# Kernel tuning notes

Hardware: AMD Instinct MI355X
Metric: run time of the kernel (lower is better)

The kernel has to match this reference:

```python
import jax, jax.numpy as jnp
import numpy as np

N = 50000
E = 800000
HID = 128
HEADS = 3
OPH = (HID + HEADS - 1) // HEADS  # 43
MID = OPH * HEADS                 # 129
OUT = 6


def _gat_layer(x, src, dst, W, a_src, a_dst, b, heads, ch, concat, num_nodes):
    # x: [N, F_in]; W: [F_in, heads*ch]; a_src/a_dst: [heads, ch]; b: [heads*ch] or [ch]
    h = (x @ W).reshape(num_nodes, heads, ch)          # [N, H, C]
    al = jnp.einsum('nhc,hc->nh', h, a_src)            # [N, H]
    ar = jnp.einsum('nhc,hc->nh', h, a_dst)            # [N, H]
    e = jax.nn.leaky_relu(al[src] + ar[dst], 0.2)      # [E, H]
    emax = jax.ops.segment_max(e, dst, num_segments=num_nodes)
    emax = jnp.where(jnp.isfinite(emax), emax, 0.0)
    ex = jnp.exp(e - emax[dst])                        # [E, H]
    denom = jax.ops.segment_sum(ex, dst, num_segments=num_nodes)
    alpha = ex / (denom[dst] + 1e-16)                  # [E, H]
    msg = h[src] * alpha[:, :, None]                   # [E, H, C]
    out = jax.ops.segment_sum(msg, dst, num_segments=num_nodes)  # [N, H, C]
    out = out.reshape(num_nodes, heads * ch) if concat else out.mean(axis=1)
    return out + b


def setup_inputs() -> dict:
    key = jax.random.key(0)
    ks = jax.random.split(key, 16)
    x = jax.random.normal(ks[0], (N, HID), dtype=jnp.float32)
    edge_index = jax.random.randint(ks[1], (2, E), 0, N, dtype=jnp.int64)
    s = 0.1
    return {
        'x': x, 'edge_index': edge_index,
        'W0': jax.random.normal(ks[2], (HID, HEADS * OPH), jnp.float32) * s,
        'a0s': jax.random.normal(ks[3], (HEADS, OPH), jnp.float32) * s,
        'a0d': jax.random.normal(ks[4], (HEADS, OPH), jnp.float32) * s,
        'b0': jnp.zeros((HEADS * OPH,), jnp.float32),
        'W1': jax.random.normal(ks[5], (MID, HEADS * OPH), jnp.float32) * s,
        'a1s': jax.random.normal(ks[6], (HEADS, OPH), jnp.float32) * s,
        'a1d': jax.random.normal(ks[7], (HEADS, OPH), jnp.float32) * s,
        'b1': jnp.zeros((HEADS * OPH,), jnp.float32),
        'W2': jax.random.normal(ks[8], (MID, OUT), jnp.float32) * s,
        'a2s': jax.random.normal(ks[9], (1, OUT), jnp.float32) * s,
        'a2d': jax.random.normal(ks[10], (1, OUT), jnp.float32) * s,
        'b2': jnp.zeros((OUT,), jnp.float32),
    }


def reference(x, edge_index, W0, a0s, a0d, b0, W1, a1s, a1d, b1, W2, a2s, a2d, b2):
    # add self loops (GATConv add_self_loops=True)
    loops = jnp.arange(N, dtype=edge_index.dtype)
    src = jnp.concatenate([edge_index[0], loops])
    dst = jnp.concatenate([edge_index[1], loops])
    h = _gat_layer(x, src, dst, W0, a0s, a0d, b0, HEADS, OPH, True, N)
    h = jax.nn.leaky_relu(h, 0.2)
    h = _gat_layer(h, src, dst, W1, a1s, a1d, b1, HEADS, OPH, True, N)
    h = jax.nn.leaky_relu(h, 0.2)
    out = _gat_layer(h, src, dst, W2, a2s, a2d, b2, 1, OUT, False, N)
    return out
```

## Files before the change

### kernel.cpp

```cpp
#include <hip/hip_runtime.h>

#define N_NODES 50000
#define N_EDGES 800000
#define ET (N_EDGES + N_NODES)
#define MID 129
#define OUTC 6
#define NB 196
#define CT 4096

typedef _Float16 half2v __attribute__((ext_vector_type(2)));
typedef _Float16 half8  __attribute__((ext_vector_type(8)));
typedef float    floatx4 __attribute__((ext_vector_type(4)));

__device__ __forceinline__ float lrelu(float x) { return fmaxf(x, 0.2f * x); }


__global__ void ccount_kernel(const int* __restrict__ dst, int* __restrict__ ccnt) {
    __shared__ int lh[NB];
    for (int i = threadIdx.x; i < NB; i += 256) lh[i] = 0;
    __syncthreads();
    int base = blockIdx.x * CT;
#pragma unroll 4
    for (int j = 0; j < CT; j += 256) {
        int e = base + j + threadIdx.x;
        if (e < ET) {
            int d = (e < N_EDGES) ? dst[e] : (e - N_EDGES);
            atomicAdd(&lh[d >> 8], 1);
        }
    }
    __syncthreads();
    for (int i = threadIdx.x; i < NB; i += 256) {
        int v = lh[i];
        if (v) atomicAdd(&ccnt[i], v);
    }
}

__global__ void cscan_kernel(const int* __restrict__ ccnt, int* __restrict__ cbase,
                             int* __restrict__ ccur) {
    __shared__ int buf[256];
    int t = threadIdx.x;
    buf[t] = (t < NB) ? ccnt[t] : 0;
    __syncthreads();
    for (int off = 1; off < 256; off <<= 1) {
        int v = (t >= off) ? buf[t - off] : 0;
        __syncthreads();
        buf[t] += v;
        __syncthreads();
    }
    int excl = t ? buf[t - 1] : 0;
    if (t < NB) { cbase[t] = excl; ccur[t] = excl; }
    if (t == NB - 1) cbase[NB] = buf[t];
}

__global__ void cscatter_kernel(const int* __restrict__ src, const int* __restrict__ dst,
                                int* __restrict__ ccur, unsigned int* __restrict__ cval) {
    __shared__ unsigned int staged[CT];
    __shared__ int lh[NB], lex[NB], lcur[NB], lgb[NB];
    __shared__ int sbuf[256];
    int tid = threadIdx.x;
    for (int i = tid; i < NB; i += 256) lh[i] = 0;
    __syncthreads();
    int base = blockIdx.x * CT;
    unsigned int myv[16];
    int myb[16];
    int myn = 0;
#pragma unroll
    for (int j = 0; j < 16; ++j) {
        int e = base + j * 256 + tid;
        if (e < ET) {
            int s, d;
            if (e < N_EDGES) { s = src[e]; d = dst[e]; }
            else             { s = d = e - N_EDGES; }
            int b = d >> 8;
            myv[j] = ((unsigned)b << 24) | ((unsigned)(d & 255) << 16) | (unsigned)s;
            myb[j] = b;
            atomicAdd(&lh[b], 1);
            myn = j + 1;
        }
    }
    __syncthreads();
    sbuf[tid] = (tid < NB) ? lh[tid] : 0;
    __syncthreads();
    for (int off = 1; off < 256; off <<= 1) {
        int v = (tid >= off) ? sbuf[tid - off] : 0;
        __syncthreads();
        sbuf[tid] += v;
        __syncthreads();
    }
    if (tid < NB) {
        int excl = tid ? sbuf[tid - 1] : 0;
        lex[tid] = excl;
        lcur[tid] = excl;
    }
    __syncthreads();
    for (int j = 0; j < myn; ++j) {
        int p = atomicAdd(&lcur[myb[j]], 1);
        staged[p] = myv[j];
    }
    __syncthreads();
    if (tid < NB) {
        int c = lh[tid];
        lgb[tid] = c ? atomicAdd(&ccur[tid], c) : 0;
    }
    __syncthreads();
    int tot = ET - base; if (tot > CT) tot = CT;
    for (int i = tid; i < tot; i += 256) {
        unsigned int v = staged[i];
        int b = v >> 24;
        cval[lgb[b] + (i - lex[b])] = v;
    }
}

__global__ __launch_bounds__(512)
void fine_kernel(const unsigned int* __restrict__ cval, const int* __restrict__ cbase,
                 int* __restrict__ rowp, unsigned short* __restrict__ csr_src) {
    __shared__ int h[256], cur[256], sb[256];
    int b = blockIdx.x;
    int beg = cbase[b], end = cbase[b + 1];
    int t = threadIdx.x;
    if (t < 256) h[t] = 0;
    __syncthreads();
    for (int i = beg + t; i < end; i += 512)
        atomicAdd(&h[(cval[i] >> 16) & 255], 1);
    __syncthreads();
    if (t < 256) sb[t] = h[t];
    __syncthreads();
    for (int off = 1; off < 256; off <<= 1) {
        int v = 0;
        if (t < 256 && t >= off) v = sb[t - off];
        __syncthreads();
        if (t < 256) sb[t] += v;
        __syncthreads();
    }
    if (t < 256) {
        int excl = t ? sb[t - 1] : 0;
        cur[t] = excl;
        int dstv = (b << 8) + t;
        if (dstv <= N_NODES) rowp[dstv] = beg + excl;
    }
    __syncthreads();
    for (int i = beg + t; i < end; i += 512) {
        unsigned int v = cval[i];
        int low = (v >> 16) & 255;
        int p = atomicAdd(&cur[low], 1);
        csr_src[beg + p] = (unsigned short)(v & 0xFFFFu);
    }
}

__global__ void padw_kernel(const float* __restrict__ W0, const float* __restrict__ a0s,
                            const float* __restrict__ a0d, const float* __restrict__ W1,
                            const float* __restrict__ a1s, const float* __restrict__ a1d,
                            _Float16* __restrict__ Wt0, _Float16* __restrict__ Wt1,
                            float* __restrict__ w128row1) {
    const int SEG = 144 * 128;
    int i = blockIdx.x * blockDim.x + threadIdx.x;
    if (i < 2 * SEG) {
        int l = i / SEG;
        int ii = i - l * SEG;
        int n = ii >> 7, k = ii & 127;
        const float* W = l ? W1 : W0;
        const float* as = l ? a1s : a0s;
        const float* ad = l ? a1d : a0d;
        float v = 0.f;
        if (n < 129) v = W[k * MID + n];
        else if (n < 132) {
            int h = n - 129;
            float sum = 0.f;
            for (int c = 0; c < 43; ++c) sum += W[k * MID + 43 * h + c] * as[43 * h + c];
            v = sum;
        } else if (n < 135) {
            int h = n - 132;
            float sum = 0.f;
            for (int c = 0; c < 43; ++c) sum += W[k * MID + 43 * h + c] * ad[43 * h + c];
            v = sum;
        }
        (l ? Wt1 : Wt0)[ii] = (_Float16)v;
    } else if (i < 2 * SEG + 144) {
        int n = i - 2 * SEG;
        float v = 0.f;
        if (n < 129) v = W1[128 * MID + n];
        else if (n < 132) {
            int h = n - 129;
            float sum = 0.f;
            for (int c = 0; c < 43; ++c) sum += W1[128 * MID + 43 * h + c] * a1s[43 * h + c];
            v = sum;
        } else if (n < 135) {
            int h = n - 132;
            float sum = 0.f;
            for (int c = 0; c < 43; ++c) sum += W1[128 * MID + 43 * h + c] * a1d[43 * h + c];
            v = sum;
        }
        w128row1[n] = v;
    }
}

template <bool SRC32, bool RANK1>
__global__ __launch_bounds__(256)
void gemm_mfma_kernel(const float* __restrict__ X32, const _Float16* __restrict__ Xh,
                      const float* __restrict__ Xl,
                      const _Float16* __restrict__ Wt, const float* __restrict__ w128,
                      _Float16* __restrict__ Hm16, float* __restrict__ Hl,
                      float* __restrict__ al4, float* __restrict__ ar4) {
    int wave = threadIdx.x >> 6, lane = threadIdx.x & 63;
    int mt = blockIdx.x * 4 + wave;
    if (mt * 16 >= N_NODES) return;
    int t = lane & 15, quad = lane >> 4;
    int row0 = mt * 16;

    half8 af[4];
    if (SRC32) {
        const float* arow = X32 + ((size_t)(row0 + t) << 7) + quad * 8;
#pragma unroll
        for (int kt = 0; kt < 4; ++kt) {
            float4 a0 = *(const float4*)(arow + kt * 32);
            float4 a1 = *(const float4*)(arow + kt * 32 + 4);
            half8 h;
            h[0] = (_Float16)a0.x; h[1] = (_Float16)a0.y;
            h[2] = (_Float16)a0.z; h[3] = (_Float16)a0.w;
            h[4] = (_Float16)a1.x; h[5] = (_Float16)a1.y;
            h[6] = (_Float16)a1.z; h[7] = (_Float16)a1.w;
            af[kt] = h;
        }
    } else {
        const _Float16* arow = Xh + ((size_t)(row0 + t) << 7) + quad * 8;
#pragma unroll
        for (int kt = 0; kt < 4; ++kt) af[kt] = *(const half8*)(arow + kt * 32);
    }

    floatx4 acc[3];
#pragma unroll
    for (int nt = 0; nt < 3; ++nt) {
        int ntile = blockIdx.y * 3 + nt;
        const _Float16* brow = Wt + ((size_t)(ntile * 16 + t) << 7) + quad * 8;
        floatx4 a = {0.f, 0.f, 0.f, 0.f};
#pragma unroll
        for (int kt = 0; kt < 4; ++kt) {
            half8 b = *(const half8*)(brow + kt * 32);
            a = __builtin_amdgcn_mfma_f32_16x16x32_f16(af[kt], b, a, 0, 0, 0);
        }
        acc[nt] = a;
    }

#pragma unroll
    for (int r = 0; r < 4; ++r) {
        int row = row0 + quad * 4 + r;
        float xl = RANK1 ? Xl[row] : 0.f;
#pragma unroll
        for (int nt = 0; nt < 3; ++nt) {
            int n = (blockIdx.y * 3 + nt) * 16 + t;
            float v = acc[nt][r];
            if (RANK1) v += xl * w128[n];
            if (n < 128) {
                Hm16[((size_t)row << 7) + n] = (_Float16)v;
            } else if (n == 128) {
                Hl[row] = v;
            } else if (n < 132) {
                al4[row * 4 + (n - 129)] = v;
            } else if (n < 135) {
                ar4[row * 4 + (n - 132)] = v;
            }
        }
    }
}

template <bool ACT, bool L2EPI>
__global__ void agg129_kernel(const _Float16* __restrict__ Hm16, const float* __restrict__ Hl,
                              const float* __restrict__ al4, const float* __restrict__ ar4,
                              const int* __restrict__ rowp, const unsigned short* __restrict__ srcs,
                              const float* __restrict__ bias, _Float16* __restrict__ Omh,
                              float* __restrict__ Ol,
                              const float* __restrict__ W2, const float* __restrict__ a2s,
                              const float* __restrict__ a2d, float* __restrict__ H2,
                              float* __restrict__ al2, float* __restrict__ ar2) {
    __shared__ float4 exs[4][4][17];
    int lane = threadIdx.x & 63;
    int wv   = threadIdx.x >> 6;
    int qd   = lane >> 4;
    int q    = lane & 15;
    int wid  = ((blockIdx.x * 4 + wv) << 2) + qd;
    bool active = wid < N_NODES;
    int widc = active ? wid : 0;

    int beg = 0, end = 0;
    if (active) { beg = rowp[wid]; end = rowp[wid + 1]; }
    float4 arv = *(const float4*)(ar4 + (size_t)widc * 4);
    float ard0 = arv.x, ard1 = arv.y, ard2 = arv.z;

    int cb = 8 * q;
    bool bm0[8], bm1[8];
#pragma unroll
    for (int j = 0; j < 8; ++j) {
        bm0[j] = (cb + j) < 43;
        bm1[j] = (cb + j) < 86;
    }
    unsigned selv[4];
#pragma unroll
    for (int p = 0; p < 4; ++p) {
        int c0 = cb + 2 * p, c1 = c0 + 1;
        int l0 = (c0 < 43) ? 4 : (c0 < 86) ? 6 : 0;
        int l1 = (c1 < 43) ? 4 : (c1 < 86) ? 6 : 0;
        selv[p] = (unsigned)l0 | ((unsigned)(l0 + 1) << 8) |
                  ((unsigned)l1 << 16) | ((unsigned)(l1 + 1) << 24);
    }

    float accv[8];
#pragma unroll
    for (int j = 0; j < 8; ++j) accv[j] = 0.f;
    float acc128 = 0.f;
    float s0 = 0.f, s1 = 0.f, s2 = 0.f;
    float4* exq = exs[wv][qd];

    for (int base = beg; base < end; base += 16) {
        int i = base + q;
        float e0 = 0.f, e1 = 0.f, e2 = 0.f;
        int s = 0;
        if (i < end) {
            s = (int)srcs[i];
            float4 av = *(const float4*)(al4 + (size_t)s * 4);
            e0 = __expf(lrelu(av.x + ard0));
            e1 = __expf(lrelu(av.y + ard1));
            e2 = __expf(lrelu(av.z + ard2));
            s0 += e0; s1 += e1; s2 += e2;
        }
        exq[q] = make_float4(e0, e1, e2, __int_as_float(s));
        int cnt = end - base; if (cnt > 16) cnt = 16;
        for (int t = 0; t < cnt; ++t) {
            float4 ed = exq[t];
            int ss = __float_as_int(ed.w);
            half8 hv = *(const half8*)(Hm16 + ((size_t)ss << 7) + cb);
            unsigned p01 = __builtin_bit_cast(unsigned, __builtin_amdgcn_cvt_pkrtz(ed.x, ed.y));
            unsigned p2z = __builtin_bit_cast(unsigned, __builtin_amdgcn_cvt_pkrtz(ed.z, ed.z));
            if (q == 0) acc128 += ed.z * Hl[ss];
#pragma unroll
            for (int p = 0; p < 4; ++p) {
                unsigned wp = __builtin_amdgcn_perm(p01, p2z, selv[p]);
                half2v w2 = __builtin_bit_cast(half2v, wp);
                accv[2 * p]     += (float)w2[0] * (float)hv[2 * p];
                accv[2 * p + 1] += (float)w2[1] * (float)hv[2 * p + 1];
            }
        }
    }
#pragma unroll
    for (int off = 1; off < 16; off <<= 1) {
        s0 += __shfl_xor(s0, off, 64);
        s1 += __shfl_xor(s1, off, 64);
        s2 += __shfl_xor(s2, off, 64);
    }
    float d0 = 1.f / (s0 + 1e-16f);
    float d1 = 1.f / (s1 + 1e-16f);
    float d2 = 1.f / (s2 + 1e-16f);

    float4 bv0 = *(const float4*)(bias + cb);
    float4 bv1 = *(const float4*)(bias + cb + 4);
    float bb[8] = {bv0.x, bv0.y, bv0.z, bv0.w, bv1.x, bv1.y, bv1.z, bv1.w};
    float o[8];
#pragma unroll
    for (int j = 0; j < 8; ++j) {
        float dv = bm0[j] ? d0 : (bm1[j] ? d1 : d2);
        o[j] = accv[j] * dv + bb[j];
        if (ACT) o[j] = lrelu(o[j]);
    }
    float o128 = 0.f;
    if (q == 0) {
        o128 = acc128 * d2 + bias[128];
        if (ACT) o128 = lrelu(o128);
    }
    if (!L2EPI) {
        if (active) {
            half8 oh;
#pragma unroll
            for (int j = 0; j < 8; ++j) oh[j] = (_Float16)o[j];
            *(half8*)(Omh + ((size_t)wid << 7) + cb) = oh;
            if (q == 0) Ol[wid] = o128;
        }
    } else {
        float pr[OUTC];
#pragma unroll
        for (int c = 0; c < OUTC; ++c) pr[c] = 0.f;
#pragma unroll
        for (int j = 0; j < 8; ++j) {
            const float* wr = W2 + (cb + j) * OUTC;
            float ov = o[j];
#pragma unroll
            for (int c = 0; c < OUTC; ++c) pr[c] += ov * wr[c];
        }
        if (q == 0) {
#pragma unroll
            for (int c = 0; c < OUTC; ++c) pr[c] += o128 * W2[128 * OUTC + c];
        }
#pragma unroll
        for (int off = 1; off < 16; off <<= 1)
#pragma unroll
            for (int c = 0; c < OUTC; ++c) pr[c] += __shfl_xor(pr[c], off, 64);
        if (active && q == 0) {
            float sl = 0.f, sr = 0.f;
#pragma unroll
            for (int c = 0; c < OUTC; ++c) {
                H2[wid * OUTC + c] = pr[c];
                sl += pr[c] * a2s[c];
                sr += pr[c] * a2d[c];
            }
            al2[wid] = sl;
            ar2[wid] = sr;
        }
    }
}

__global__ void agg6_kernel(const float* __restrict__ H2, const float* __restrict__ al2,
                            const float* __restrict__ ar2, const int* __restrict__ rowp,
                            const unsigned short* __restrict__ srcs, const float* __restrict__ b2,
                            float* __restrict__ out) {
    __shared__ float2 exs[4][8][9];
    int lane = threadIdx.x & 63;
    int wv   = threadIdx.x >> 6;
    int g8   = lane >> 3;
    int c    = lane & 7;
    int wid  = ((blockIdx.x * 4 + wv) << 3) + g8;
    bool active = wid < N_NODES;
    int widc = active ? wid : 0;
    int beg = 0, end = 0;
    if (active) { beg = rowp[wid]; end = rowp[wid + 1]; }
    float ard = ar2[widc];
    int cc = (c < OUTC) ? c : 0;
    float ssum = 0.f, acc = 0.f;
    float2* exq = exs[wv][g8];
    for (int base = beg; base < end; base += 8) {
        int i = base + c;
        float ex = 0.f;
        int s = 0;
        if (i < end) {
            s = (int)srcs[i];
            ex = __expf(lrelu(al2[s] + ard));
            ssum += ex;
        }
        exq[c] = make_float2(ex, __int_as_float(s));
        int cnt = end - base; if (cnt > 8) cnt = 8;
        for (int t = 0; t < cnt; ++t) {
            float2 ed = exq[t];
            int ss = __float_as_int(ed.y);
            acc += ed.x * H2[ss * OUTC + cc];
        }
    }
#pragma unroll
    for (int off = 1; off < 8; off <<= 1) ssum += __shfl_xor(ssum, off, 64);
    float dinv = 1.f / (ssum + 1e-16f);
    if (active && c < OUTC) out[(size_t)wid * OUTC + c] = acc * dinv + b2[c];
}


extern "C" void kernel_launch(void* const* d_in, const int* in_sizes, int n_in,
                              void* d_out, int out_size, void* d_ws, size_t ws_size,
                              hipStream_t stream) {
    const float* x   = (const float*)d_in[0];
    const int*   ei  = (const int*)d_in[1];
    const float* W0  = (const float*)d_in[2];
    const float* a0s = (const float*)d_in[3];
    const float* a0d = (const float*)d_in[4];
    const float* b0  = (const float*)d_in[5];
    const float* W1  = (const float*)d_in[6];
    const float* a1s = (const float*)d_in[7];
    const float* a1d = (const float*)d_in[8];
    const float* b1  = (const float*)d_in[9];
    const float* W2  = (const float*)d_in[10];
    const float* a2s = (const float*)d_in[11];
    const float* a2d = (const float*)d_in[12];
    const float* b2  = (const float*)d_in[13];
    float* out = (float*)d_out;

    char* p = (char*)d_ws;
    auto take = [&](size_t bytes) -> void* {
        void* r = (void*)p;
        p += (bytes + 255) & ~(size_t)255;
        return r;
    };
    int*            ccnt     = (int*)take((size_t)NB * 4);
    int*            cbase    = (int*)take((size_t)(NB + 1) * 4);
    int*            ccur     = (int*)take((size_t)NB * 4);
    unsigned int*   cval     = (unsigned int*)take((size_t)ET * 4);
    int*            rowp     = (int*)take((size_t)(N_NODES + 1) * 4);
    unsigned short* csr_src  = (unsigned short*)take((size_t)ET * 2);
    float*          al4      = (float*)take((size_t)N_NODES * 4 * 4);
    float*          ar4      = (float*)take((size_t)N_NODES * 4 * 4);
    _Float16*       Hm16     = (_Float16*)take((size_t)N_NODES * 128 * 2);
    _Float16*       Omh      = (_Float16*)take((size_t)N_NODES * 128 * 2);
    float*          Hl       = (float*)take((size_t)N_NODES * 4);
    float*          Ol       = (float*)take((size_t)N_NODES * 4);
    _Float16*       Wt0      = (_Float16*)take((size_t)144 * 128 * 2);
    _Float16*       Wt1      = (_Float16*)take((size_t)144 * 128 * 2);
    float*          w128row1 = (float*)take((size_t)144 * 4);
    float*          H2       = (float*)take((size_t)N_NODES * OUTC * 4);
    float*          al2      = (float*)take((size_t)N_NODES * 4);
    float*          ar2      = (float*)take((size_t)N_NODES * 4);

    const int* esrc = ei;
    const int* edst = ei + N_EDGES;

    hipMemsetAsync(ccnt, 0, (size_t)NB * 4, stream);
    const int cgrid = (ET + CT - 1) / CT;
    ccount_kernel<<<cgrid, 256, 0, stream>>>(edst, ccnt);
    cscan_kernel<<<1, 256, 0, stream>>>(ccnt, cbase, ccur);
    cscatter_kernel<<<cgrid, 256, 0, stream>>>(esrc, edst, ccur, cval);
    fine_kernel<<<NB, 512, 0, stream>>>(cval, cbase, rowp, csr_src);

    padw_kernel<<<(2 * 144 * 128 + 144 + 255) / 256, 256, 0, stream>>>(
        W0, a0s, a0d, W1, a1s, a1d, Wt0, Wt1, w128row1);

    const dim3 gemm_grid((N_NODES / 16 + 3) / 4, 3);
    const int  agg129_grid = (N_NODES + 15) / 16;
    const int  agg6_grid   = (N_NODES + 31) / 32;

    gemm_mfma_kernel<true, false><<<gemm_grid, 256, 0, stream>>>(
        x, (const _Float16*)nullptr, Ol, Wt0, w128row1, Hm16, Hl, al4, ar4);
    agg129_kernel<true, false><<<agg129_grid, 256, 0, stream>>>(
        Hm16, Hl, al4, ar4, rowp, csr_src, b0, Omh, Ol,
        nullptr, nullptr, nullptr, nullptr, nullptr, nullptr);

    gemm_mfma_kernel<false, true><<<gemm_grid, 256, 0, stream>>>(
        (const float*)nullptr, Omh, Ol, Wt1, w128row1, Hm16, Hl, al4, ar4);
    agg129_kernel<true, true><<<agg129_grid, 256, 0, stream>>>(
        Hm16, Hl, al4, ar4, rowp, csr_src, b1, (_Float16*)nullptr, (float*)nullptr,
        W2, a2s, a2d, H2, al2, ar2);

    agg6_kernel<<<agg6_grid, 256, 0, stream>>>(H2, al2, ar2, rowp, csr_src, b2, out);
}
```

Baseline: 280.5 us.

## Fuse independent preprocessing kernels and unroll aggregation gather loops

Merges the edge-count kernel with the weight-padding kernel, and the coarse scatter kernel with the first-layer GEMM, into single launches whose blocks branch on block index, so independent work shares a launch and can overlap. This removes two kernel launches and the serialization between them. It also unrolls the per-edge gather loops in the 129-wide and 6-wide aggregation kernels by 4 and 2, issuing several neighbor loads before the math to raise memory-level parallelism. The cost is more registers and shared memory in the fused kernels, which may lower occupancy.

```diff
diff --git a/kernel.cpp b/kernel.cpp
--- a/kernel.cpp
+++ b/kernel.cpp
@@ -7,6 +7,9 @@
 #define OUTC 6
 #define NB 196
 #define CT 4096
+#define CGRID ((ET + CT - 1) / CT)
+#define MTB ((N_NODES / 16 + 3) / 4)
+#define PADW_BLOCKS ((2 * 144 * 128 + 144 + 255) / 256)
 
 typedef _Float16 half2v __attribute__((ext_vector_type(2)));
 typedef _Float16 half8  __attribute__((ext_vector_type(8)));
@@ -14,146 +17,12 @@
 
 __device__ __forceinline__ float lrelu(float x) { return fmaxf(x, 0.2f * x); }
 
-
-__global__ void ccount_kernel(const int* __restrict__ dst, int* __restrict__ ccnt) {
-    __shared__ int lh[NB];
-    for (int i = threadIdx.x; i < NB; i += 256) lh[i] = 0;
-    __syncthreads();
-    int base = blockIdx.x * CT;
-#pragma unroll 4
-    for (int j = 0; j < CT; j += 256) {
-        int e = base + j + threadIdx.x;
-        if (e < ET) {
-            int d = (e < N_EDGES) ? dst[e] : (e - N_EDGES);
-            atomicAdd(&lh[d >> 8], 1);
-        }
-    }
-    __syncthreads();
-    for (int i = threadIdx.x; i < NB; i += 256) {
-        int v = lh[i];
-        if (v) atomicAdd(&ccnt[i], v);
-    }
-}
-
-__global__ void cscan_kernel(const int* __restrict__ ccnt, int* __restrict__ cbase,
-                             int* __restrict__ ccur) {
-    __shared__ int buf[256];
-    int t = threadIdx.x;
-    buf[t] = (t < NB) ? ccnt[t] : 0;
-    __syncthreads();
-    for (int off = 1; off < 256; off <<= 1) {
-        int v = (t >= off) ? buf[t - off] : 0;
-        __syncthreads();
-        buf[t] += v;
-        __syncthreads();
-    }
-    int excl = t ? buf[t - 1] : 0;
-    if (t < NB) { cbase[t] = excl; ccur[t] = excl; }
-    if (t == NB - 1) cbase[NB] = buf[t];
-}
-
-__global__ void cscatter_kernel(const int* __restrict__ src, const int* __restrict__ dst,
-                                int* __restrict__ ccur, unsigned int* __restrict__ cval) {
-    __shared__ unsigned int staged[CT];
-    __shared__ int lh[NB], lex[NB], lcur[NB], lgb[NB];
-    __shared__ int sbuf[256];
-    int tid = threadIdx.x;
-    for (int i = tid; i < NB; i += 256) lh[i] = 0;
-    __syncthreads();
-    int base = blockIdx.x * CT;
-    unsigned int myv[16];
-    int myb[16];
-    int myn = 0;
-#pragma unroll
-    for (int j = 0; j < 16; ++j) {
-        int e = base + j * 256 + tid;
-        if (e < ET) {
-            int s, d;
-            if (e < N_EDGES) { s = src[e]; d = dst[e]; }
-            else             { s = d = e - N_EDGES; }
-            int b = d >> 8;
-            myv[j] = ((unsigned)b << 24) | ((unsigned)(d & 255) << 16) | (unsigned)s;
-            myb[j] = b;
-            atomicAdd(&lh[b], 1);
-            myn = j + 1;
-        }
-    }
-    __syncthreads();
-    sbuf[tid] = (tid < NB) ? lh[tid] : 0;
-    __syncthreads();
-    for (int off = 1; off < 256; off <<= 1) {
-        int v = (tid >= off) ? sbuf[tid - off] : 0;
-        __syncthreads();
-        sbuf[tid] += v;
-        __syncthreads();
-    }
-    if (tid < NB) {
-        int excl = tid ? sbuf[tid - 1] : 0;
-        lex[tid] = excl;
-        lcur[tid] = excl;
-    }
-    __syncthreads();
-    for (int j = 0; j < myn; ++j) {
-        int p = atomicAdd(&lcur[myb[j]], 1);
-        staged[p] = myv[j];
-    }
-    __syncthreads();
-    if (tid < NB) {
-        int c = lh[tid];
-        lgb[tid] = c ? atomicAdd(&ccur[tid], c) : 0;
-    }
-    __syncthreads();
-    int tot = ET - base; if (tot > CT) tot = CT;
-    for (int i = tid; i < tot; i += 256) {
-        unsigned int v = staged[i];
-        int b = v >> 24;
-        cval[lgb[b] + (i - lex[b])] = v;
-    }
-}
-
-__global__ __launch_bounds__(512)
-void fine_kernel(const unsigned int* __restrict__ cval, const int* __restrict__ cbase,
-                 int* __restrict__ rowp, unsigned short* __restrict__ csr_src) {
-    __shared__ int h[256], cur[256], sb[256];
-    int b = blockIdx.x;
-    int beg = cbase[b], end = cbase[b + 1];
-    int t = threadIdx.x;
-    if (t < 256) h[t] = 0;
-    __syncthreads();
-    for (int i = beg + t; i < end; i += 512)
-        atomicAdd(&h[(cval[i] >> 16) & 255], 1);
-    __syncthreads();
-    if (t < 256) sb[t] = h[t];
-    __syncthreads();
-    for (int off = 1; off < 256; off <<= 1) {
-        int v = 0;
-        if (t < 256 && t >= off) v = sb[t - off];
-        __syncthreads();
-        if (t < 256) sb[t] += v;
-        __syncthreads();
-    }
-    if (t < 256) {
-        int excl = t ? sb[t - 1] : 0;
-        cur[t] = excl;
-        int dstv = (b << 8) + t;
-        if (dstv <= N_NODES) rowp[dstv] = beg + excl;
-    }
-    __syncthreads();
-    for (int i = beg + t; i < end; i += 512) {
-        unsigned int v = cval[i];
-        int low = (v >> 16) & 255;
-        int p = atomicAdd(&cur[low], 1);
-        csr_src[beg + p] = (unsigned short)(v & 0xFFFFu);
-    }
-}
-
-__global__ void padw_kernel(const float* __restrict__ W0, const float* __restrict__ a0s,
-                            const float* __restrict__ a0d, const float* __restrict__ W1,
-                            const float* __restrict__ a1s, const float* __restrict__ a1d,
-                            _Float16* __restrict__ Wt0, _Float16* __restrict__ Wt1,
-                            float* __restrict__ w128row1) {
+__device__ __forceinline__ void padw_body(int i, const float* __restrict__ W0,
+                                          const float* __restrict__ a0s, const float* __restrict__ a0d,
+                                          const float* __restrict__ W1, const float* __restrict__ a1s,
+                                          const float* __restrict__ a1d, _Float16* __restrict__ Wt0,
+                                          _Float16* __restrict__ Wt1, float* __restrict__ w128row1) {
     const int SEG = 144 * 128;
-    int i = blockIdx.x * blockDim.x + threadIdx.x;
     if (i < 2 * SEG) {
         int l = i / SEG;
         int ii = i - l * SEG;
@@ -174,7 +43,7 @@
             for (int c = 0; c < 43; ++c) sum += W[k * MID + 43 * h + c] * ad[43 * h + c];
             v = sum;
         }
-        (l ? Wt1 : Wt0)[ii] = (_Float16)v;
+        (l ? Wt1 : Wt0)[i - l * SEG] = (_Float16)v;
     } else if (i < 2 * SEG + 144) {
         int n = i - 2 * SEG;
         float v = 0.f;
@@ -194,15 +63,65 @@
     }
 }
 
+__global__ __launch_bounds__(256)
+void fused_count_padw_kernel(const int* __restrict__ dst, int* __restrict__ ccnt,
+                             const float* __restrict__ W0, const float* __restrict__ a0s,
+                             const float* __restrict__ a0d, const float* __restrict__ W1,
+                             const float* __restrict__ a1s, const float* __restrict__ a1d,
+                             _Float16* __restrict__ Wt0, _Float16* __restrict__ Wt1,
+                             float* __restrict__ w128row1) {
+    if ((int)blockIdx.x < CGRID) {
+        __shared__ int lh[NB];
+        for (int i = threadIdx.x; i < NB; i += 256) lh[i] = 0;
+        __syncthreads();
+        int base = blockIdx.x * CT;
+#pragma unroll 4
+        for (int j = 0; j < CT; j += 256) {
+            int e = base + j + threadIdx.x;
+            if (e < ET) {
+                int d = (e < N_EDGES) ? dst[e] : (e - N_EDGES);
+                atomicAdd(&lh[d >> 8], 1);
+            }
+        }
+        __syncthreads();
+        for (int i = threadIdx.x; i < NB; i += 256) {
+            int v = lh[i];
+            if (v) atomicAdd(&ccnt[i], v);
+        }
+    } else {
+        int i = ((int)blockIdx.x - CGRID) * 256 + threadIdx.x;
+        padw_body(i, W0, a0s, a0d, W1, a1s, a1d, Wt0, Wt1, w128row1);
+    }
+}
+
+__global__ void cscan_kernel(const int* __restrict__ ccnt, int* __restrict__ cbase,
+                             int* __restrict__ ccur) {
+    __shared__ int buf[256];
+    int t = threadIdx.x;
+    buf[t] = (t < NB) ? ccnt[t] : 0;
+    __syncthreads();
+    for (int off = 1; off < 256; off <<= 1) {
+        int v = (t >= off) ? buf[t - off] : 0;
+        __syncthreads();
+        buf[t] += v;
+        __syncthreads();
+    }
+    int excl = t ? buf[t - 1] : 0;
+    if (t < NB) { cbase[t] = excl; ccur[t] = excl; }
+    if (t == NB - 1) cbase[NB] = buf[t];
+}
+
 template <bool SRC32, bool RANK1>
-__global__ __launch_bounds__(256)
-void gemm_mfma_kernel(const float* __restrict__ X32, const _Float16* __restrict__ Xh,
-                      const float* __restrict__ Xl,
-                      const _Float16* __restrict__ Wt, const float* __restrict__ w128,
-                      _Float16* __restrict__ Hm16, float* __restrict__ Hl,
-                      float* __restrict__ al4, float* __restrict__ ar4) {
-    int wave = threadIdx.x >> 6, lane = threadIdx.x & 63;
-    int mt = blockIdx.x * 4 + wave;
+__device__ __forceinline__ void gemm_body(int mtb, int nyb, int tid,
+                                          const float* __restrict__ X32,
+                                          const _Float16* __restrict__ Xh,
+                                          const float* __restrict__ Xl,
+                                          const _Float16* __restrict__ Wt,
+                                          const float* __restrict__ w128,
+                                          _Float16* __restrict__ Hm16, float* __restrict__ Hl,
+                                          float* __restrict__ al4, float* __restrict__ ar4) {
+    int wave = tid >> 6, lane = tid & 63;
+    int mt = mtb * 4 + wave;
     if (mt * 16 >= N_NODES) return;
     int t = lane & 15, quad = lane >> 4;
     int row0 = mt * 16;
@@ -230,7 +149,7 @@
     floatx4 acc[3];
 #pragma unroll
     for (int nt = 0; nt < 3; ++nt) {
-        int ntile = blockIdx.y * 3 + nt;
+        int ntile = nyb * 3 + nt;
         const _Float16* brow = Wt + ((size_t)(ntile * 16 + t) << 7) + quad * 8;
         floatx4 a = {0.f, 0.f, 0.f, 0.f};
 #pragma unroll
@@ -247,7 +166,7 @@
         float xl = RANK1 ? Xl[row] : 0.f;
 #pragma unroll
         for (int nt = 0; nt < 3; ++nt) {
-            int n = (blockIdx.y * 3 + nt) * 16 + t;
+            int n = (nyb * 3 + nt) * 16 + t;
             float v = acc[nt][r];
             if (RANK1) v += xl * w128[n];
             if (n < 128) {
@@ -261,6 +180,122 @@
             }
         }
     }
+}
+
+__global__ __launch_bounds__(256)
+void fused_scatter_gemm0_kernel(const int* __restrict__ src, const int* __restrict__ dst,
+                                int* __restrict__ ccur, unsigned int* __restrict__ cval,
+                                const float* __restrict__ X32, const _Float16* __restrict__ Wt0,
+                                _Float16* __restrict__ Hm16, float* __restrict__ Hl,
+                                float* __restrict__ al4, float* __restrict__ ar4) {
+    if ((int)blockIdx.x < CGRID) {
+        __shared__ unsigned int staged[CT];
+        __shared__ int lh[NB], lex[NB], lcur[NB], lgb[NB];
+        __shared__ int sbuf[256];
+        int tid = threadIdx.x;
+        for (int i = tid; i < NB; i += 256) lh[i] = 0;
+        __syncthreads();
+        int base = blockIdx.x * CT;
+        unsigned int myv[16];
+        int myb[16];
+        int myn = 0;
+#pragma unroll
+        for (int j = 0; j < 16; ++j) {
+            int e = base + j * 256 + tid;
+            if (e < ET) {
+                int s, d;
+                if (e < N_EDGES) { s = src[e]; d = dst[e]; }
+                else             { s = d = e - N_EDGES; }
+                int b = d >> 8;
+                myv[j] = ((unsigned)b << 24) | ((unsigned)(d & 255) << 16) | (unsigned)s;
+                myb[j] = b;
+                atomicAdd(&lh[b], 1);
+                myn = j + 1;
+            }
+        }
+        __syncthreads();
+        sbuf[tid] = (tid < NB) ? lh[tid] : 0;
+        __syncthreads();
+        for (int off = 1; off < 256; off <<= 1) {
+            int v = (tid >= off) ? sbuf[tid - off] : 0;
+            __syncthreads();
+            sbuf[tid] += v;
+            __syncthreads();
+        }
+        if (tid < NB) {
+            int excl = tid ? sbuf[tid - 1] : 0;
+            lex[tid] = excl;
+            lcur[tid] = excl;
+        }
+        __syncthreads();
+        for (int j = 0; j < myn; ++j) {
+            int p = atomicAdd(&lcur[myb[j]], 1);
+            staged[p] = myv[j];
+        }
+        __syncthreads();
+        if (tid < NB) {
+            int c = lh[tid];
+            lgb[tid] = c ? atomicAdd(&ccur[tid], c) : 0;
+        }
+        __syncthreads();
+        int tot = ET - base; if (tot > CT) tot = CT;
+        for (int i = tid; i < tot; i += 256) {
+            unsigned int v = staged[i];
+            int b = v >> 24;
+            cval[lgb[b] + (i - lex[b])] = v;
+        }
+    } else {
+        int b = (int)blockIdx.x - CGRID;
+        int nyb = b / MTB;
+        int mtb = b - nyb * MTB;
+        gemm_body<true, false>(mtb, nyb, threadIdx.x, X32, nullptr, nullptr,
+                               Wt0, nullptr, Hm16, Hl, al4, ar4);
+    }
+}
+
+__global__ __launch_bounds__(512)
+void fine_kernel(const unsigned int* __restrict__ cval, const int* __restrict__ cbase,
+                 int* __restrict__ rowp, unsigned short* __restrict__ csr_src) {
+    __shared__ int h[256], cur[256], sb[256];
+    int b = blockIdx.x;
+    int beg = cbase[b], end = cbase[b + 1];
+    int t = threadIdx.x;
+    if (t < 256) h[t] = 0;
+    __syncthreads();
+    for (int i = beg + t; i < end; i += 512)
+        atomicAdd(&h[(cval[i] >> 16) & 255], 1);
+    __syncthreads();
+    if (t < 256) sb[t] = h[t];
+    __syncthreads();
+    for (int off = 1; off < 256; off <<= 1) {
+        int v = 0;
+        if (t < 256 && t >= off) v = sb[t - off];
+        __syncthreads();
+        if (t < 256) sb[t] += v;
+        __syncthreads();
+    }
+    if (t < 256) {
+        int excl = t ? sb[t - 1] : 0;
+        cur[t] = excl;
+        int dstv = (b << 8) + t;
+        if (dstv <= N_NODES) rowp[dstv] = beg + excl;
+    }
+    __syncthreads();
+    for (int i = beg + t; i < end; i += 512) {
+        unsigned int v = cval[i];
+        int low = (v >> 16) & 255;
+        int p = atomicAdd(&cur[low], 1);
+        csr_src[beg + p] = (unsigned short)(v & 0xFFFFu);
+    }
+}
+
+__global__ __launch_bounds__(256)
+void gemm1_kernel(const _Float16* __restrict__ Xh, const float* __restrict__ Xl,
+                  const _Float16* __restrict__ Wt, const float* __restrict__ w128,
+                  _Float16* __restrict__ Hm16, float* __restrict__ Hl,
+                  float* __restrict__ al4, float* __restrict__ ar4) {
+    gemm_body<false, true>(blockIdx.x, blockIdx.y, threadIdx.x, nullptr, Xh, Xl,
+                           Wt, w128, Hm16, Hl, al4, ar4);
 }
 
 template <bool ACT, bool L2EPI>
@@ -324,13 +359,44 @@
         }
         exq[q] = make_float4(e0, e1, e2, __int_as_float(s));
         int cnt = end - base; if (cnt > 16) cnt = 16;
-        for (int t = 0; t < cnt; ++t) {
+        int t = 0;
+        for (; t + 3 < cnt; t += 4) {
+            float4 ed[4];
+            int sx[4];
+            half8 hv[4];
+#pragma unroll
+            for (int u = 0; u < 4; ++u) ed[u] = exq[t + u];
+#pragma unroll
+            for (int u = 0; u < 4; ++u) {
+                sx[u] = __float_as_int(ed[u].w);
+                hv[u] = *(const half8*)(Hm16 + ((size_t)sx[u] << 7) + cb);
+            }
+            if (q == 0) {
+                acc128 += ed[0].z * Hl[sx[0]];
+                acc128 += ed[1].z * Hl[sx[1]];
+                acc128 += ed[2].z * Hl[sx[2]];
+                acc128 += ed[3].z * Hl[sx[3]];
+            }
+#pragma unroll
+            for (int u = 0; u < 4; ++u) {
+                unsigned p01 = __builtin_bit_cast(unsigned, __builtin_amdgcn_cvt_pkrtz(ed[u].x, ed[u].y));
+                unsigned p2z = __builtin_bit_cast(unsigned, __builtin_amdgcn_cvt_pkrtz(ed[u].z, ed[u].z));
+#pragma unroll
+                for (int p = 0; p < 4; ++p) {
+                    unsigned wp = __builtin_amdgcn_perm(p01, p2z, selv[p]);
+                    half2v w2 = __builtin_bit_cast(half2v, wp);
+                    accv[2 * p]     += (float)w2[0] * (float)hv[u][2 * p];
+                    accv[2 * p + 1] += (float)w2[1] * (float)hv[u][2 * p + 1];
+                }
+            }
+        }
+        for (; t < cnt; ++t) {
             float4 ed = exq[t];
             int ss = __float_as_int(ed.w);
             half8 hv = *(const half8*)(Hm16 + ((size_t)ss << 7) + cb);
+            if (q == 0) acc128 += ed.z * Hl[ss];
             unsigned p01 = __builtin_bit_cast(unsigned, __builtin_amdgcn_cvt_pkrtz(ed.x, ed.y));
             unsigned p2z = __builtin_bit_cast(unsigned, __builtin_amdgcn_cvt_pkrtz(ed.z, ed.z));
-            if (q == 0) acc128 += ed.z * Hl[ss];
 #pragma unroll
             for (int p = 0; p < 4; ++p) {
                 unsigned wp = __builtin_amdgcn_perm(p01, p2z, selv[p]);
@@ -435,7 +501,17 @@
         }
         exq[c] = make_float2(ex, __int_as_float(s));
         int cnt = end - base; if (cnt > 8) cnt = 8;
-        for (int t = 0; t < cnt; ++t) {
+        int t = 0;
+        for (; t + 1 < cnt; t += 2) {
+            float2 eda = exq[t];
+            float2 edb = exq[t + 1];
+            int sa = __float_as_int(eda.y);
+            int sb = __float_as_int(edb.y);
+            float ha = H2[sa * OUTC + cc];
+            float hb = H2[sb * OUTC + cc];
+            acc += eda.x * ha + edb.x * hb;
+        }
+        if (t < cnt) {
             float2 ed = exq[t];
             int ss = __float_as_int(ed.y);
             acc += ed.x * H2[ss * OUTC + cc];
@@ -496,27 +572,23 @@
     const int* edst = ei + N_EDGES;
 
     hipMemsetAsync(ccnt, 0, (size_t)NB * 4, stream);
-    const int cgrid = (ET + CT - 1) / CT;
-    ccount_kernel<<<cgrid, 256, 0, stream>>>(edst, ccnt);
+
+    fused_count_padw_kernel<<<CGRID + PADW_BLOCKS, 256, 0, stream>>>(
+        edst, ccnt, W0, a0s, a0d, W1, a1s, a1d, Wt0, Wt1, w128row1);
     cscan_kernel<<<1, 256, 0, stream>>>(ccnt, cbase, ccur);
-    cscatter_kernel<<<cgrid, 256, 0, stream>>>(esrc, edst, ccur, cval);
+
+    fused_scatter_gemm0_kernel<<<CGRID + MTB * 3, 256, 0, stream>>>(
+        esrc, edst, ccur, cval, x, Wt0, Hm16, Hl, al4, ar4);
     fine_kernel<<<NB, 512, 0, stream>>>(cval, cbase, rowp, csr_src);
 
-    padw_kernel<<<(2 * 144 * 128 + 144 + 255) / 256, 256, 0, stream>>>(
-        W0, a0s, a0d, W1, a1s, a1d, Wt0, Wt1, w128row1);
-
-    const dim3 gemm_grid((N_NODES / 16 + 3) / 4, 3);
-    const int  agg129_grid = (N_NODES + 15) / 16;
-    const int  agg6_grid   = (N_NODES + 31) / 32;
-
-    gemm_mfma_kernel<true, false><<<gemm_grid, 256, 0, stream>>>(
-        x, (const _Float16*)nullptr, Ol, Wt0, w128row1, Hm16, Hl, al4, ar4);
+    const int agg129_grid = (N_NODES + 15) / 16;
+    const int agg6_grid   = (N_NODES + 31) / 32;
+
     agg129_kernel<true, false><<<agg129_grid, 256, 0, stream>>>(
         Hm16, Hl, al4, ar4, rowp, csr_src, b0, Omh, Ol,
         nullptr, nullptr, nullptr, nullptr, nullptr, nullptr);
 
-    gemm_mfma_kernel<false, true><<<gemm_grid, 256, 0, stream>>>(
-        (const float*)nullptr, Omh, Ol, Wt1, w128row1, Hm16, Hl, al4, ar4);
+    gemm1_kernel<<<dim3(MTB, 3), 256, 0, stream>>>(Omh, Ol, Wt1, w128row1, Hm16, Hl, al4, ar4);
     agg129_kernel<true, true><<<agg129_grid, 256, 0, stream>>>(
         Hm16, Hl, al4, ar4, rowp, csr_src, b1, (_Float16*)nullptr, (float*)nullptr,
         W2, a2s, a2d, H2, al2, ar2);
```

Result: faster. 262.3 us (-6.5%).
